# Kernel optimization log

Hardware: AMD Instinct MI355X
Metric: run time of the kernel (lower is better)

## Reference

```python
import jax, jax.numpy as jnp
import numpy as np

OUT, IN = 4096, 4096      # weight_shape
VDIM = 8                  # codebook vector_dim
CODEBOOK_SIZE = 256
LEVEL = 2                 # haar_decomposition_level
INV_SQRT2 = 0.7071067811865476


def unpack_bool(packed, shape):
    # packed: int array of bytes (values 0..255); unpack 8 bits per byte (LSB first)
    bits = (packed[:, None] >> jnp.arange(8, dtype=packed.dtype)) & 1  # [n_bytes, 8]
    return bits.reshape(shape)


def inverse_haar(c, level):
    # c: [..., n] orthonormal Haar coefficients laid out [a_L, d_L, d_{L-1}, ..., d_1]
    n = c.shape[-1]
    m = n >> level
    a = c[..., :m]
    while m < n:
        d = c[..., m:2 * m]
        even = (a + d) * INV_SQRT2
        odd = (a - d) * INV_SQRT2
        a = jnp.stack([even, odd], axis=-1).reshape(c.shape[:-1] + (2 * m,))
        m *= 2
    return a


def setup_inputs() -> dict:
    key = jax.random.key(0)
    k1, k2, k3, k4, k5 = jax.random.split(key, 5)
    x = jax.random.normal(k1, (4, 2048, IN), dtype=jnp.float32)
    codebook = jax.random.normal(k2, (CODEBOOK_SIZE, VDIM), dtype=jnp.float32)
    scales = jax.random.uniform(k5, (OUT, 1), dtype=jnp.float32)
    indices = jax.random.randint(k3, (OUT * IN // VDIM,), 0, CODEBOOK_SIZE, dtype=jnp.int32)
    signs_packed = jax.random.randint(k4, (OUT * IN // 8,), 0, 256, dtype=jnp.int32)
    return {"x": x, "codebook": codebook, "scales": scales,
            "indices": indices, "signs_packed": signs_packed}


def reference(x, codebook, scales, indices, signs_packed):
    # codebook gather -> haar-domain magnitudes, reshaped to signs_shape = weight shape
    haar_freq = codebook[indices].reshape(OUT, IN)
    # unpack sign bits and map {0,1} -> {-1,+1}
    signs = 2.0 * unpack_bool(signs_packed, (OUT, IN)).astype(haar_freq.dtype) - 1.0
    haar_freq = haar_freq * signs
    # multi-level inverse Haar wavelet along in_features
    w = inverse_haar(haar_freq, LEVEL)
    w = w * scales  # per-output-row scales
    return jnp.einsum('bsi,oi->bso', x, w)
```

## Files before the change

### kernel.cpp

```cpp
#include <hip/hip_runtime.h>
#include <hip/hip_bf16.h>

typedef unsigned short u16;
typedef unsigned int u32;
typedef float f32x4 __attribute__((ext_vector_type(4)));
typedef u16 u16x4 __attribute__((ext_vector_type(4)));
typedef u16 u16x8 __attribute__((ext_vector_type(8)));
typedef __bf16 bf16x8 __attribute__((ext_vector_type(8)));

#define OUT_DIM 4096
#define IN_DIM  4096
#define M_DIM   8192

__device__ __forceinline__ u16 f2bf(float f) {
  u32 u = __builtin_bit_cast(u32, f);
  return (u16)((u + 0x7FFFu + ((u >> 16) & 1u)) >> 16);
}

__global__ __launch_bounds__(256) void build_w_kernel(
    const float* __restrict__ codebook, const float* __restrict__ scales,
    const int* __restrict__ indices, const int* __restrict__ signs,
    u16* __restrict__ W) {
  __shared__ float c[IN_DIM];
  const int o   = blockIdx.x;
  const int tid = threadIdx.x;
  for (int g = tid; g < IN_DIM / 8; g += 256) {
    const int idx = indices[o * (IN_DIM / 8) + g];
    const int sp  = signs[o * (IN_DIM / 8) + g];
    f32x4 c0 = *(const f32x4*)&codebook[idx * 8];
    f32x4 c1 = *(const f32x4*)&codebook[idx * 8 + 4];
    float v[8] = {c0[0], c0[1], c0[2], c0[3], c1[0], c1[1], c1[2], c1[3]};
#pragma unroll
    for (int j = 0; j < 8; ++j)
      c[g * 8 + j] = ((sp >> j) & 1) ? v[j] : -v[j];
  }
  __syncthreads();
  const float scale = scales[o];
  const float S = 0.70710678118654752440f;
  for (int t = tid; t < IN_DIM / 4; t += 256) {
    float a   = c[t];
    float d1  = c[IN_DIM / 4 + t];
    float d2a = c[IN_DIM / 2 + 2 * t];
    float d2b = c[IN_DIM / 2 + 2 * t + 1];
    float e  = (a + d1) * S;
    float od = (a - d1) * S;
    u16x4 w;
    w[0] = f2bf((e  + d2a) * S * scale);
    w[1] = f2bf((e  - d2a) * S * scale);
    w[2] = f2bf((od + d2b) * S * scale);
    w[3] = f2bf((od - d2b) * S * scale);
    *(u16x4*)&W[(size_t)o * IN_DIM + 4 * t] = w;
  }
}

__global__ __launch_bounds__(256) void cvt_x_kernel(
    const float* __restrict__ X, u16* __restrict__ Xb) {
  const int stride = gridDim.x * blockDim.x;
  const int n8 = (M_DIM * IN_DIM) / 8;
  for (int i = blockIdx.x * blockDim.x + threadIdx.x; i < n8; i += stride) {
    f32x4 a = *(const f32x4*)&X[(size_t)i * 8];
    f32x4 b = *(const f32x4*)&X[(size_t)i * 8 + 4];
    u16x8 r;
    r[0] = f2bf(a[0]); r[1] = f2bf(a[1]); r[2] = f2bf(a[2]); r[3] = f2bf(a[3]);
    r[4] = f2bf(b[0]); r[5] = f2bf(b[1]); r[6] = f2bf(b[2]); r[7] = f2bf(b[3]);
    *(u16x8*)&Xb[(size_t)i * 8] = r;
  }
}

__global__ __launch_bounds__(512) void gemm_bt_kernel(
    const u16* __restrict__ A,
    const u16* __restrict__ B,
    float*     __restrict__ C) {
  constexpr int K    = IN_DIM;
  constexpr int NT   = K / 32;
  constexpr int BUFB = 32768;
  extern __shared__ char smem[];

  const int tid  = threadIdx.x;
  const int wave = tid >> 6;
  const int lane = tid & 63;

  const int swz = (blockIdx.x & 7) * 64 + (blockIdx.x >> 3);
  const int bm = (swz >> 4) * 256;
  const int bn = (swz & 15) * 256;

  const int wr  = (wave >> 2) * 128;
  const int wc  = (wave & 3) * 64;
  const int fr  = lane & 15;
  const int fkB = (lane >> 4) * 16;

  int offA[8], offB[4];
#pragma unroll
  for (int h = 0; h < 8; ++h) {
    int o = (wr + h * 16 + fr) * 64 + fkB;
    offA[h] = o ^ ((o >> 3) & 0x30);
  }
#pragma unroll
  for (int n = 0; n < 4; ++n) {
    int o = (wc + n * 16 + fr) * 64 + fkB;
    offB[n] = 16384 + (o ^ ((o >> 3) & 0x30));
  }

  const u16* srcA[2]; const u16* srcB[2];
#pragma unroll
  for (int i = 0; i < 2; ++i) {
    int d = i * 8192 + tid * 16;
    int l = d ^ ((d >> 3) & 0x30);
    int row = d >> 6;
    srcA[i] = A + (size_t)(bm + row) * K + ((l & 63) >> 1);
    srcB[i] = B + (size_t)(bn + row) * K + ((l & 63) >> 1);
  }
  const int ldsW = wave * 1024;

  f32x4 acc[8][4] = {};

  auto stageA = [&](int tt) {
    char* base = smem + (tt & 3) * BUFB + ldsW;
#pragma unroll
    for (int i = 0; i < 2; ++i)
      __builtin_amdgcn_global_load_lds(
          (const __attribute__((address_space(1))) void*)(srcA[i] + tt * 32),
          (__attribute__((address_space(3))) void*)(base + i * 8192), 16, 0, 0);
  };
  auto stageB = [&](int tt) {
    char* base = smem + (tt & 3) * BUFB + 16384 + ldsW;
#pragma unroll
    for (int i = 0; i < 2; ++i)
      __builtin_amdgcn_global_load_lds(
          (const __attribute__((address_space(1))) void*)(srcB[i] + tt * 32),
          (__attribute__((address_space(3))) void*)(base + i * 8192), 16, 0, 0);
  };

  stageA(0); stageB(0); stageA(1); stageB(1); stageA(2); stageB(2);
  asm volatile("s_waitcnt vmcnt(8)" ::: "memory");
  __builtin_amdgcn_s_barrier();

  for (int t = 0; t < NT; ++t) {
    const char* buf = smem + (t & 3) * BUFB;
    bf16x8 bfv[4], af[4];
#pragma unroll
    for (int n = 0; n < 4; ++n) bfv[n] = *(const bf16x8*)(buf + offB[n]);
#pragma unroll
    for (int m = 0; m < 4; ++m) af[m] = *(const bf16x8*)(buf + offA[m]);
    if (t + 3 < NT) stageA(t + 3);
    __builtin_amdgcn_s_barrier();
    __builtin_amdgcn_s_setprio(1);
#pragma unroll
    for (int m = 0; m < 4; ++m)
#pragma unroll
      for (int n = 0; n < 4; ++n)
        acc[m][n] = __builtin_amdgcn_mfma_f32_16x16x32_bf16(af[m], bfv[n], acc[m][n], 0, 0, 0);
    __builtin_amdgcn_s_setprio(0);
    __builtin_amdgcn_s_barrier();
#pragma unroll
    for (int m = 0; m < 4; ++m) af[m] = *(const bf16x8*)(buf + offA[4 + m]);
    if (t + 3 < NT) stageB(t + 3);
    __builtin_amdgcn_s_barrier();
    __builtin_amdgcn_s_setprio(1);
#pragma unroll
    for (int m = 0; m < 4; ++m)
#pragma unroll
      for (int n = 0; n < 4; ++n)
        acc[4 + m][n] = __builtin_amdgcn_mfma_f32_16x16x32_bf16(af[m], bfv[n], acc[4 + m][n], 0, 0, 0);
    __builtin_amdgcn_s_setprio(0);
    if (t + 3 < NT)      asm volatile("s_waitcnt vmcnt(8)" ::: "memory");
    else if (t + 2 < NT) asm volatile("s_waitcnt vmcnt(4)" ::: "memory");
    else                 asm volatile("s_waitcnt vmcnt(0)" ::: "memory");
    __builtin_amdgcn_s_barrier();
  }

#pragma unroll
  for (int h = 0; h < 8; ++h)
#pragma unroll
    for (int n = 0; n < 4; ++n) {
      const int col = bn + wc + n * 16 + fr;
#pragma unroll
      for (int j = 0; j < 4; ++j) {
        const int row = bm + wr + h * 16 + (lane >> 4) * 4 + j;
        C[(size_t)row * OUT_DIM + col] = acc[h][n][j];
      }
    }
}

extern "C" void kernel_launch(void* const* d_in, const int* in_sizes, int n_in,
                              void* d_out, int out_size, void* d_ws, size_t ws_size,
                              hipStream_t stream) {
  const float* x        = (const float*)d_in[0];
  const float* codebook = (const float*)d_in[1];
  const float* scales   = (const float*)d_in[2];
  const int*   indices  = (const int*)d_in[3];
  const int*   signs    = (const int*)d_in[4];
  float* out = (float*)d_out;

  u16* W  = (u16*)d_ws;
  u16* Xb = (u16*)d_ws + (size_t)OUT_DIM * IN_DIM;

  (void)hipFuncSetAttribute((const void*)gemm_bt_kernel,
                            hipFuncAttributeMaxDynamicSharedMemorySize, 131072);

  build_w_kernel<<<OUT_DIM, 256, 0, stream>>>(codebook, scales, indices, signs, W);
  cvt_x_kernel<<<2048, 256, 0, stream>>>(x, Xb);
  gemm_bt_kernel<<<(M_DIM / 256) * (OUT_DIM / 256), 512, 131072, stream>>>(Xb, W, out);
}
```

Before: 301.5 us.

## Software-pipeline LDS fragment reads across K-tiles with double-buffered registers

Restructures the GEMM main loop so the next K-tile's A-low and B fragments are read from LDS during the current tile's second MFMA half. Register sets alternate (ping-pong) and the loop is unrolled by two. Barriers drop from four to two per tile, and the vmcnt waits are retuned to match the new stage order. It also adds a launch_bounds occupancy hint of 2, which with this much accumulator state may force register spills or tighter allocation. The changed wait counts also risk ordering errors around the LDS ring buffer.

```diff
diff --git a/kernel.cpp b/kernel.cpp
--- a/kernel.cpp
+++ b/kernel.cpp
@@ -67,7 +67,7 @@
   }
 }
 
-__global__ __launch_bounds__(512) void gemm_bt_kernel(
+__global__ __launch_bounds__(512, 2) void gemm_bt_kernel(
     const u16* __restrict__ A,
     const u16* __restrict__ B,
     float*     __restrict__ C) {
@@ -112,8 +112,6 @@
   }
   const int ldsW = wave * 1024;
 
-  f32x4 acc[8][4] = {};
-
   auto stageA = [&](int tt) {
     char* base = smem + (tt & 3) * BUFB + ldsW;
 #pragma unroll
@@ -131,42 +129,58 @@
           (__attribute__((address_space(3))) void*)(base + i * 8192), 16, 0, 0);
   };
 
+  f32x4 acc[8][4] = {};
+  bf16x8 aloX[4], bX[4], aloY[4], bY[4], ahi[4];
+
   stageA(0); stageB(0); stageA(1); stageB(1); stageA(2); stageB(2);
   asm volatile("s_waitcnt vmcnt(8)" ::: "memory");
   __builtin_amdgcn_s_barrier();
-
-  for (int t = 0; t < NT; ++t) {
-    const char* buf = smem + (t & 3) * BUFB;
-    bf16x8 bfv[4], af[4];
-#pragma unroll
-    for (int n = 0; n < 4; ++n) bfv[n] = *(const bf16x8*)(buf + offB[n]);
-#pragma unroll
-    for (int m = 0; m < 4; ++m) af[m] = *(const bf16x8*)(buf + offA[m]);
+  {
+    const char* buf0 = smem;
+#pragma unroll
+    for (int n = 0; n < 4; ++n) bX[n]   = *(const bf16x8*)(buf0 + offB[n]);
+#pragma unroll
+    for (int m = 0; m < 4; ++m) aloX[m] = *(const bf16x8*)(buf0 + offA[m]);
+  }
+
+  auto tile = [&](int t, bf16x8 (&cA)[4], bf16x8 (&cB)[4],
+                  bf16x8 (&nA)[4], bf16x8 (&nB)[4]) {
+    const char* buf  = smem + (t & 3) * BUFB;
+    const char* bufn = smem + ((t + 1) & 3) * BUFB;
     if (t + 3 < NT) stageA(t + 3);
+#pragma unroll
+    for (int m = 0; m < 4; ++m) ahi[m] = *(const bf16x8*)(buf + offA[4 + m]);
+    __builtin_amdgcn_s_setprio(1);
+#pragma unroll
+    for (int m = 0; m < 4; ++m)
+#pragma unroll
+      for (int n = 0; n < 4; ++n)
+        acc[m][n] = __builtin_amdgcn_mfma_f32_16x16x32_bf16(cA[m], cB[n], acc[m][n], 0, 0, 0);
+    __builtin_amdgcn_s_setprio(0);
+    if (t + 3 < NT)       asm volatile("s_waitcnt vmcnt(6)" ::: "memory");
+    else if (t + 3 == NT) asm volatile("s_waitcnt vmcnt(4)" ::: "memory");
+    else if (t + 2 == NT) asm volatile("s_waitcnt vmcnt(0)" ::: "memory");
     __builtin_amdgcn_s_barrier();
+    if (t + 3 < NT) stageB(t + 3);
+    if (t + 1 < NT) {
+#pragma unroll
+      for (int n = 0; n < 4; ++n) nB[n] = *(const bf16x8*)(bufn + offB[n]);
+#pragma unroll
+      for (int m = 0; m < 4; ++m) nA[m] = *(const bf16x8*)(bufn + offA[m]);
+    }
     __builtin_amdgcn_s_setprio(1);
 #pragma unroll
     for (int m = 0; m < 4; ++m)
 #pragma unroll
       for (int n = 0; n < 4; ++n)
-        acc[m][n] = __builtin_amdgcn_mfma_f32_16x16x32_bf16(af[m], bfv[n], acc[m][n], 0, 0, 0);
+        acc[4 + m][n] = __builtin_amdgcn_mfma_f32_16x16x32_bf16(ahi[m], cB[n], acc[4 + m][n], 0, 0, 0);
     __builtin_amdgcn_s_setprio(0);
     __builtin_amdgcn_s_barrier();
-#pragma unroll
-    for (int m = 0; m < 4; ++m) af[m] = *(const bf16x8*)(buf + offA[4 + m]);
-    if (t + 3 < NT) stageB(t + 3);
-    __builtin_amdgcn_s_barrier();
-    __builtin_amdgcn_s_setprio(1);
-#pragma unroll
-    for (int m = 0; m < 4; ++m)
-#pragma unroll
-      for (int n = 0; n < 4; ++n)
-        acc[4 + m][n] = __builtin_amdgcn_mfma_f32_16x16x32_bf16(af[m], bfv[n], acc[4 + m][n], 0, 0, 0);
-    __builtin_amdgcn_s_setprio(0);
-    if (t + 3 < NT)      asm volatile("s_waitcnt vmcnt(8)" ::: "memory");
-    else if (t + 2 < NT) asm volatile("s_waitcnt vmcnt(4)" ::: "memory");
-    else                 asm volatile("s_waitcnt vmcnt(0)" ::: "memory");
-    __builtin_amdgcn_s_barrier();
+  };
+
+  for (int t = 0; t < NT; t += 2) {
+    tile(t,     aloX, bX, aloY, bY);
+    tile(t + 1, aloY, bY, aloX, bX);
   }
 
 #pragma unroll
```

After: 295.7 us. About the same (-2.0%).
